# Performance work log

Measured on AMD Instinct MI355X. Metric: run time of the kernel, lower is better.

The kernel has to match this reference:

```python
import jax, jax.numpy as jnp
import numpy as np
from jax import lax

B, CIN, COUT, K, H, W, SDIM = 16, 256, 256, 3, 64, 64, 512


def setup_inputs() -> dict:
    key = jax.random.key(0)
    k1, k2, k3, k4 = jax.random.split(key, 4)
    return {
        "x": jax.random.normal(k1, (B, CIN, H, W), jnp.float32),
        "style": jax.random.normal(k2, (B, SDIM), jnp.float32),
        "weight": jax.random.normal(k3, (COUT, CIN, K, K), jnp.float32),
        "style_w": jax.random.normal(k4, (SDIM, CIN), jnp.float32) * (1.0 / np.sqrt(SDIM)),
        "style_b": jnp.zeros((CIN,), jnp.float32),
    }


def reference(x, style, weight, style_w, style_b):
    b, cin, h, w_sz = x.shape
    cout, _, k, _ = weight.shape
    mod_scale = 1.0 / np.sqrt(cin * k * k)
    # style projection: [B, CIN]
    s = style @ style_w + style_b
    # modulate: [B, COUT, CIN, K, K]
    wmod = weight[None] * s[:, None, :, None, None] * mod_scale
    # demodulate over (cin, kh, kw)
    demod = lax.rsqrt(jnp.sum(wmod * wmod, axis=(2, 3, 4)) + 1e-8)  # [B, COUT]
    wmod = wmod * demod[:, :, None, None, None]
    # per-sample conv (groups=batch equivalent) via vmap
    def conv1(xb, wb):
        # xb: [CIN, H, W], wb: [COUT, CIN, K, K]
        return lax.conv_general_dilated(
            xb[None], wb, window_strides=(1, 1), padding=[(1, 1), (1, 1)],
            dimension_numbers=("NCHW", "OIHW", "NCHW"))[0]
    return jax.vmap(conv1)(x, wmod)  # [B, COUT, H, W]
```

## Files before the change

### kernel.cpp

```cpp
#include <hip/hip_runtime.h>
#include <hip/hip_bf16.h>

#define BB 16
#define CIN 256
#define COUT 256
#define HH 64
#define WW 64
#define SDIM 512

typedef __attribute__((ext_vector_type(8))) short bf16x8;
typedef __attribute__((ext_vector_type(4))) float f32x4;

static __device__ __forceinline__ short f2bf(float v) {
    __hip_bfloat16 h = __float2bfloat16(v);
    return *reinterpret_cast<short*>(&h);
}

__global__ void style_proj_kernel(const float* __restrict__ style,
                                  const float* __restrict__ style_w,
                                  const float* __restrict__ style_b,
                                  float* __restrict__ s) {
    __shared__ float red[3][64];
    int l    = threadIdx.x & 63;
    int part = threadIdx.x >> 6;
    int ci   = blockIdx.x * 64 + l;
    int b    = blockIdx.y;
    float acc = 0.f;
    const float* st = style + b * SDIM + part * (SDIM / 4);
    const float* W  = style_w + (size_t)(part * (SDIM / 4)) * CIN + ci;
#pragma unroll 4
    for (int k = 0; k < SDIM / 4; ++k) acc += st[k] * W[(size_t)k * CIN];
    if (part) red[part - 1][l] = acc;
    __syncthreads();
    if (part == 0)
        s[b * CIN + ci] = acc + red[0][l] + red[1][l] + red[2][l] + style_b[ci];
}

__global__ void wprep_kernel(const float* __restrict__ w,
                             __hip_bfloat16* __restrict__ wT,
                             float* __restrict__ wsq) {
    int co = blockIdx.x;
    int ci = threadIdx.x;
    const float* wp = w + ((size_t)co * CIN + ci) * 9;
    float acc = 0.f;
#pragma unroll
    for (int k = 0; k < 9; ++k) {
        float v = wp[k];
        acc += v * v;
        wT[((size_t)co * 9 + k) * CIN + ci] = __float2bfloat16(v);
    }
    wsq[co * CIN + ci] = acc;
}

__global__ void demod_kernel(const float* __restrict__ wsq,
                             const float* __restrict__ s,
                             float* __restrict__ demod) {
    int b    = blockIdx.y;
    int co   = blockIdx.x * 4 + (threadIdx.x >> 6);
    int lane = threadIdx.x & 63;
    float acc = 0.f;
#pragma unroll
    for (int j = 0; j < CIN / 64; ++j) {
        int ci = j * 64 + lane;
        float sv = s[b * CIN + ci];
        acc += wsq[co * CIN + ci] * sv * sv;
    }
#pragma unroll
    for (int off = 32; off > 0; off >>= 1)
        acc += __shfl_down(acc, off, 64);
    if (lane == 0)
        demod[b * COUT + co] = rsqrtf(acc * (1.0f / (CIN * 9)) + 1e-8f);
}

__global__ void xmod_kernel(const float* __restrict__ x,
                            const float* __restrict__ s,
                            __hip_bfloat16* __restrict__ xm) {
    int px = threadIdx.x & 63;
    int y  = blockIdx.x * 4 + (threadIdx.x >> 6);
    int g  = blockIdx.y;
    int b  = blockIdx.z;
    const float* xp = x + (((size_t)(b * CIN + g * 8)) * HH + y) * WW + px;
    const float4* sp = (const float4*)(s + b * CIN + g * 8);
    float4 s0 = sp[0], s1 = sp[1];
    float sv[8] = {s0.x, s0.y, s0.z, s0.w, s1.x, s1.y, s1.z, s1.w};
    bf16x8 v;
#pragma unroll
    for (int c = 0; c < 8; ++c) v[c] = f2bf(xp[(size_t)c * (HH * WW)] * sv[c]);
    *(bf16x8*)(xm + ((((size_t)(b * 32 + g)) * HH + y) * WW + px) * 8) = v;
}

__device__ __forceinline__ void stage_dma(__hip_bfloat16* xs,
                                          const __hip_bfloat16* __restrict__ xm,
                                          int b, int cc, int Y0, int lane,
                                          int wave) {
#pragma unroll
    for (int i = 0; i < 10; ++i) {
        int u = wave * 10 + i;
        int r = u >> 2, q = u & 3;
        int y = Y0 - 1 + r;
        if ((unsigned)y < (unsigned)HH) {
            __hip_bfloat16* dst = xs + (u * 66 + 1) * 8;
            const __hip_bfloat16* src =
                xm + ((((size_t)(b * 32 + cc * 4 + q)) * HH + y) * WW + lane) * 8;
            __builtin_amdgcn_global_load_lds(
                (const __attribute__((address_space(1))) void*)src,
                (__attribute__((address_space(3))) void*)dst, 16, 0, 0);
        }
    }
}

__device__ __forceinline__ void load_af(bf16x8 (&af)[2][9],
                                        const __hip_bfloat16* __restrict__ wb,
                                        int cc) {
#pragma unroll
    for (int k = 0; k < 9; ++k) {
        af[0][k] = *(const bf16x8*)(wb + (size_t)k * CIN + cc * 32);
        af[1][k] = *(const bf16x8*)(wb + (size_t)(16 * 9 + k) * CIN + cc * 32);
    }
}

__global__ __launch_bounds__(256, 2) void conv_mfma_kernel(
    const __hip_bfloat16* __restrict__ xm, const __hip_bfloat16* __restrict__ wT,
    const float* __restrict__ wsq, const float* __restrict__ s,
    float* __restrict__ out) {
    __shared__ __hip_bfloat16 xs[40 * 66 * 8];
    __shared__ float dls[64];

    int tid  = threadIdx.x;
    int lane = tid & 63;
    int wave = tid >> 6;
    int wco  = wave >> 1;
    int rp   = wave & 1;
    int n    = lane & 15;
    int quad = lane >> 4;

    int Y0  = blockIdx.x * 8;
    int co0 = blockIdx.y * 64;
    int b   = blockIdx.z;

    const bf16x8 zv = (bf16x8){0, 0, 0, 0, 0, 0, 0, 0};
    if (tid < 80) {
        int rowq = tid >> 1, col = (tid & 1) * 65;
        *(bf16x8*)(&xs[(rowq * 66 + col) * 8]) = zv;
    }
    if (Y0 == 0) {
        for (int c = tid; c < 264; c += 256)
            *(bf16x8*)(&xs[c * 8]) = zv;
    }
    if (Y0 + 8 == HH) {
        for (int c = tid; c < 264; c += 256)
            *(bf16x8*)(&xs[(36 * 66 + c) * 8]) = zv;
    }

    stage_dma(xs, xm, b, 0, Y0, lane, wave);

    const __hip_bfloat16* wb =
        wT + ((size_t)(co0 + wco * 32 + n) * 9) * CIN + quad * 8;
    bf16x8 af[2][9];
    load_af(af, wb, 0);

    {
        int colco = tid >> 2, part = tid & 3;
        float dacc = 0.f;
        const float* wrow = wsq + (size_t)(co0 + colco) * CIN + part * 64;
        const float* srow = s + b * CIN + part * 64;
#pragma unroll 8
        for (int i = 0; i < 64; ++i) {
            float sv = srow[i];
            dacc += wrow[i] * sv * sv;
        }
        dacc += __shfl_down(dacc, 2, 64);
        dacc += __shfl_down(dacc, 1, 64);
        if (part == 0)
            dls[colco] = rsqrtf(dacc * (1.0f / (CIN * 9)) + 1e-8f);
    }

    f32x4 acc[4][2][4];
#pragma unroll
    for (int wr = 0; wr < 4; ++wr)
#pragma unroll
        for (int m = 0; m < 2; ++m)
#pragma unroll
            for (int j = 0; j < 4; ++j) acc[wr][m][j] = (f32x4){0.f, 0.f, 0.f, 0.f};

    __syncthreads();

    for (int cc = 0; cc < 8; ++cc) {
#pragma unroll
        for (int r6 = 0; r6 < 6; ++r6) {
            int rr = rp * 4 + r6;
#pragma unroll
            for (int dx = 0; dx < 3; ++dx) {
#pragma unroll
                for (int j = 0; j < 4; ++j) {
                    bf16x8 bv = *(const bf16x8*)(
                        xs + ((rr * 4 + quad) * 66 + j * 16 + n + dx) * 8);
#pragma unroll
                    for (int wr = 0; wr < 4; ++wr) {
                        int dy = r6 - wr;
                        if (dy >= 0 && dy <= 2) {
                            acc[wr][0][j] = __builtin_amdgcn_mfma_f32_16x16x32_bf16(
                                af[0][dy * 3 + dx], bv, acc[wr][0][j], 0, 0, 0);
                            acc[wr][1][j] = __builtin_amdgcn_mfma_f32_16x16x32_bf16(
                                af[1][dy * 3 + dx], bv, acc[wr][1][j], 0, 0, 0);
                        }
                    }
                }
            }
        }
        if (cc < 7) {
            __syncthreads();
            stage_dma(xs, xm, b, cc + 1, Y0, lane, wave);
            load_af(af, wb, cc + 1);
            __syncthreads();
        }
    }

    const float ms = 1.0f / 48.0f;
#pragma unroll
    for (int wr = 0; wr < 4; ++wr) {
        int gy = Y0 + rp * 4 + wr;
#pragma unroll
        for (int m = 0; m < 2; ++m) {
            int cl = wco * 32 + m * 16 + quad * 4;
            int cobase = co0 + cl;
            float d0 = dls[cl + 0] * ms;
            float d1 = dls[cl + 1] * ms;
            float d2 = dls[cl + 2] * ms;
            float d3 = dls[cl + 3] * ms;
#pragma unroll
            for (int j = 0; j < 4; ++j) {
                int gx = j * 16 + n;
                size_t o = ((size_t)(b * COUT + cobase) * HH + gy) * WW + gx;
                out[o]                       = acc[wr][m][j][0] * d0;
                out[o + (size_t)HH * WW]     = acc[wr][m][j][1] * d1;
                out[o + (size_t)2 * HH * WW] = acc[wr][m][j][2] * d2;
                out[o + (size_t)3 * HH * WW] = acc[wr][m][j][3] * d3;
            }
        }
    }
}

__device__ __forceinline__ void stage_tile(
    __hip_bfloat16* __restrict__ xsb,
    const float* __restrict__ x, const float* __restrict__ s,
    int b, int cc, int Y0, int lane, int wave) {
#pragma unroll
    for (int i = 0; i < 6; ++i) {
        int u = wave * 6 + i;
        int r = u >> 2, quad = u & 3;
        int y = Y0 - 1 + r;
        bf16x8 wv = (bf16x8){0, 0, 0, 0, 0, 0, 0, 0};
        if ((unsigned)y < (unsigned)HH) {
            const float* base =
                x + (((size_t)(b * CIN + cc * 32 + quad * 8)) * HH + y) * WW + lane;
            const float4* sp = (const float4*)(s + b * CIN + cc * 32 + quad * 8);
            float4 s0 = sp[0], s1 = sp[1];
            float sv[8] = {s0.x, s0.y, s0.z, s0.w, s1.x, s1.y, s1.z, s1.w};
#pragma unroll
            for (int c = 0; c < 8; ++c)
                wv[c] = f2bf(base[(size_t)c * (HH * WW)] * sv[c]);
        }
        *(bf16x8*)(xsb + (((r * 4 + quad) * 66) + 1 + lane) * 8) = wv;
        if (lane < 2) {
            bf16x8 z = (bf16x8){0, 0, 0, 0, 0, 0, 0, 0};
            *(bf16x8*)(xsb + (((r * 4 + quad) * 66) + lane * 65) * 8) = z;
        }
    }
}

__global__ __launch_bounds__(256, 2) void conv_mfma_fb(
    const float* __restrict__ x, const __hip_bfloat16* __restrict__ wT,
    const float* __restrict__ s, const float* __restrict__ demod,
    float* __restrict__ out) {
    __shared__ __hip_bfloat16 xs[2][6 * 4 * 66 * 8];

    int tid  = threadIdx.x;
    int lane = tid & 63;
    int wave = tid >> 6;
    int wco  = wave >> 1;
    int rp   = wave & 1;
    int n    = lane & 15;
    int quad = lane >> 4;

    int Y0  = blockIdx.x * 4;
    int co0 = blockIdx.y * 64;
    int b   = blockIdx.z;

    f32x4 acc[2][2][4];
#pragma unroll
    for (int wr = 0; wr < 2; ++wr)
#pragma unroll
        for (int m = 0; m < 2; ++m)
#pragma unroll
            for (int j = 0; j < 4; ++j) acc[wr][m][j] = (f32x4){0.f, 0.f, 0.f, 0.f};

    const __hip_bfloat16* wb =
        wT + ((size_t)(co0 + wco * 32 + n) * 9) * CIN + quad * 8;

    stage_tile(xs[0], x, s, b, 0, Y0, lane, wave);
    __syncthreads();

    for (int cc = 0; cc < 8; ++cc) {
        int cur = cc & 1;
        if (cc < 7) stage_tile(xs[cur ^ 1], x, s, b, cc + 1, Y0, lane, wave);

        bf16x8 af[2][9];
#pragma unroll
        for (int k = 0; k < 9; ++k) {
            af[0][k] = *(const bf16x8*)(wb + ((size_t)k) * CIN + cc * 32);
            af[1][k] = *(const bf16x8*)(wb + ((size_t)(16 * 9 + k)) * CIN + cc * 32);
        }

        const __hip_bfloat16* xb = xs[cur];
#pragma unroll
        for (int r4 = 0; r4 < 4; ++r4) {
            int rr = rp * 2 + r4;
#pragma unroll
            for (int dx = 0; dx < 3; ++dx) {
#pragma unroll
                for (int j = 0; j < 4; ++j) {
                    bf16x8 bv = *(const bf16x8*)(
                        xb + (((rr * 4 + quad) * 66) + j * 16 + n + dx) * 8);
                    if (r4 <= 2) {
                        acc[0][0][j] = __builtin_amdgcn_mfma_f32_16x16x32_bf16(
                            af[0][r4 * 3 + dx], bv, acc[0][0][j], 0, 0, 0);
                        acc[0][1][j] = __builtin_amdgcn_mfma_f32_16x16x32_bf16(
                            af[1][r4 * 3 + dx], bv, acc[0][1][j], 0, 0, 0);
                    }
                    if (r4 >= 1) {
                        acc[1][0][j] = __builtin_amdgcn_mfma_f32_16x16x32_bf16(
                            af[0][(r4 - 1) * 3 + dx], bv, acc[1][0][j], 0, 0, 0);
                        acc[1][1][j] = __builtin_amdgcn_mfma_f32_16x16x32_bf16(
                            af[1][(r4 - 1) * 3 + dx], bv, acc[1][1][j], 0, 0, 0);
                    }
                }
            }
        }
        __syncthreads();
    }

    const float ms = 1.0f / 48.0f;
#pragma unroll
    for (int wr = 0; wr < 2; ++wr) {
        int gy = Y0 + rp * 2 + wr;
#pragma unroll
        for (int m = 0; m < 2; ++m) {
            int cobase = co0 + wco * 32 + m * 16 + quad * 4;
            float d0 = demod[b * COUT + cobase + 0] * ms;
            float d1 = demod[b * COUT + cobase + 1] * ms;
            float d2 = demod[b * COUT + cobase + 2] * ms;
            float d3 = demod[b * COUT + cobase + 3] * ms;
#pragma unroll
            for (int j = 0; j < 4; ++j) {
                int gx = j * 16 + n;
                size_t o = ((size_t)(b * COUT + cobase) * HH + gy) * WW + gx;
                out[o]                       = acc[wr][m][j][0] * d0;
                out[o + (size_t)HH * WW]     = acc[wr][m][j][1] * d1;
                out[o + (size_t)2 * HH * WW] = acc[wr][m][j][2] * d2;
                out[o + (size_t)3 * HH * WW] = acc[wr][m][j][3] * d3;
            }
        }
    }
}

extern "C" void kernel_launch(void* const* d_in, const int* in_sizes, int n_in,
                              void* d_out, int out_size, void* d_ws, size_t ws_size,
                              hipStream_t stream) {
    const float* x       = (const float*)d_in[0];
    const float* style   = (const float*)d_in[1];
    const float* weight  = (const float*)d_in[2];
    const float* style_w = (const float*)d_in[3];
    const float* style_b = (const float*)d_in[4];
    float* out = (float*)d_out;

    float* s     = (float*)d_ws;
    float* wsq   = s + BB * CIN;
    float* demod = wsq + COUT * CIN;
    __hip_bfloat16* wT = (__hip_bfloat16*)(demod + BB * COUT);
    __hip_bfloat16* xm = wT + (size_t)COUT * 9 * CIN;

    size_t need = (size_t)(BB * CIN + COUT * CIN + BB * COUT) * sizeof(float) +
                  (size_t)COUT * 9 * CIN * sizeof(__hip_bfloat16) +
                  (size_t)BB * CIN * HH * WW * sizeof(__hip_bfloat16);

    style_proj_kernel<<<dim3(CIN / 64, BB), 256, 0, stream>>>(style, style_w,
                                                              style_b, s);
    wprep_kernel<<<COUT, CIN, 0, stream>>>(weight, wT, wsq);

    if (ws_size >= need) {
        xmod_kernel<<<dim3(HH / 4, CIN / 8, BB), 256, 0, stream>>>(x, s, xm);
        conv_mfma_kernel<<<dim3(HH / 8, COUT / 64, BB), 256, 0, stream>>>(
            xm, wT, wsq, s, out);
    } else {
        demod_kernel<<<dim3(COUT / 4, BB), 256, 0, stream>>>(wsq, s, demod);
        conv_mfma_fb<<<dim3(HH / 4, COUT / 64, BB), 256, 0, stream>>>(
            x, wT, s, demod, out);
    }
}
```

Baseline: 216.7 us.

## Read pre-padded activations straight from global memory instead of LDS staging

The xmod kernel now writes a zero-padded 66x66 bf16 layout, so the conv kernel can read B fragments directly from global memory (through cache) instead of staging tiles into LDS with two barriers per channel chunk. The style projection and weight prep kernels are merged into one launch, and weight fragments are loaded at the top of each chunk. This removes LDS traffic and block-level syncs, but each fragment is now a global or L2 load with longer latency and no explicit overlap with the MFMAs.

```diff
diff --git a/kernel.cpp b/kernel.cpp
--- a/kernel.cpp
+++ b/kernel.cpp
@@ -11,45 +11,51 @@
 typedef __attribute__((ext_vector_type(8))) short bf16x8;
 typedef __attribute__((ext_vector_type(4))) float f32x4;
 
+#define XROW 66
+#define XPLANE (XROW * XROW)
+
 static __device__ __forceinline__ short f2bf(float v) {
     __hip_bfloat16 h = __float2bfloat16(v);
     return *reinterpret_cast<short*>(&h);
 }
 
-__global__ void style_proj_kernel(const float* __restrict__ style,
-                                  const float* __restrict__ style_w,
-                                  const float* __restrict__ style_b,
-                                  float* __restrict__ s) {
+__global__ void prep_kernel(const float* __restrict__ style,
+                            const float* __restrict__ style_w,
+                            const float* __restrict__ style_b,
+                            const float* __restrict__ weight,
+                            float* __restrict__ s,
+                            __hip_bfloat16* __restrict__ wT,
+                            float* __restrict__ wsq) {
     __shared__ float red[3][64];
-    int l    = threadIdx.x & 63;
-    int part = threadIdx.x >> 6;
-    int ci   = blockIdx.x * 64 + l;
-    int b    = blockIdx.y;
-    float acc = 0.f;
-    const float* st = style + b * SDIM + part * (SDIM / 4);
-    const float* W  = style_w + (size_t)(part * (SDIM / 4)) * CIN + ci;
+    int bx = blockIdx.x;
+    if (bx < 64) {
+        int l    = threadIdx.x & 63;
+        int part = threadIdx.x >> 6;
+        int ci   = (bx & 3) * 64 + l;
+        int b    = bx >> 2;
+        float acc = 0.f;
+        const float* st = style + b * SDIM + part * (SDIM / 4);
+        const float* W  = style_w + (size_t)(part * (SDIM / 4)) * CIN + ci;
 #pragma unroll 4
-    for (int k = 0; k < SDIM / 4; ++k) acc += st[k] * W[(size_t)k * CIN];
-    if (part) red[part - 1][l] = acc;
-    __syncthreads();
-    if (part == 0)
-        s[b * CIN + ci] = acc + red[0][l] + red[1][l] + red[2][l] + style_b[ci];
-}
-
-__global__ void wprep_kernel(const float* __restrict__ w,
-                             __hip_bfloat16* __restrict__ wT,
-                             float* __restrict__ wsq) {
-    int co = blockIdx.x;
-    int ci = threadIdx.x;
-    const float* wp = w + ((size_t)co * CIN + ci) * 9;
-    float acc = 0.f;
-#pragma unroll
-    for (int k = 0; k < 9; ++k) {
-        float v = wp[k];
-        acc += v * v;
-        wT[((size_t)co * 9 + k) * CIN + ci] = __float2bfloat16(v);
-    }
-    wsq[co * CIN + ci] = acc;
+        for (int k = 0; k < SDIM / 4; ++k) acc += st[k] * W[(size_t)k * CIN];
+        if (part) red[part - 1][l] = acc;
+        __syncthreads();
+        if (part == 0)
+            s[b * CIN + ci] =
+                acc + red[0][l] + red[1][l] + red[2][l] + style_b[ci];
+    } else {
+        int co = bx - 64;
+        int ci = threadIdx.x;
+        const float* wp = weight + ((size_t)co * CIN + ci) * 9;
+        float acc = 0.f;
+#pragma unroll
+        for (int k = 0; k < 9; ++k) {
+            float v = wp[k];
+            acc += v * v;
+            wT[((size_t)co * 9 + k) * CIN + ci] = __float2bfloat16(v);
+        }
+        wsq[co * CIN + ci] = acc;
+    }
 }
 
 __global__ void demod_kernel(const float* __restrict__ wsq,
@@ -76,46 +82,30 @@
                             const float* __restrict__ s,
                             __hip_bfloat16* __restrict__ xm) {
     int px = threadIdx.x & 63;
-    int y  = blockIdx.x * 4 + (threadIdx.x >> 6);
-    int g  = blockIdx.y;
-    int b  = blockIdx.z;
-    const float* xp = x + (((size_t)(b * CIN + g * 8)) * HH + y) * WW + px;
-    const float4* sp = (const float4*)(s + b * CIN + g * 8);
-    float4 s0 = sp[0], s1 = sp[1];
-    float sv[8] = {s0.x, s0.y, s0.z, s0.w, s1.x, s1.y, s1.z, s1.w};
-    bf16x8 v;
-#pragma unroll
-    for (int c = 0; c < 8; ++c) v[c] = f2bf(xp[(size_t)c * (HH * WW)] * sv[c]);
-    *(bf16x8*)(xm + ((((size_t)(b * 32 + g)) * HH + y) * WW + px) * 8) = v;
-}
-
-__device__ __forceinline__ void stage_dma(__hip_bfloat16* xs,
-                                          const __hip_bfloat16* __restrict__ xm,
-                                          int b, int cc, int Y0, int lane,
-                                          int wave) {
-#pragma unroll
-    for (int i = 0; i < 10; ++i) {
-        int u = wave * 10 + i;
-        int r = u >> 2, q = u & 3;
-        int y = Y0 - 1 + r;
-        if ((unsigned)y < (unsigned)HH) {
-            __hip_bfloat16* dst = xs + (u * 66 + 1) * 8;
-            const __hip_bfloat16* src =
-                xm + ((((size_t)(b * 32 + cc * 4 + q)) * HH + y) * WW + lane) * 8;
-            __builtin_amdgcn_global_load_lds(
-                (const __attribute__((address_space(1))) void*)src,
-                (__attribute__((address_space(3))) void*)dst, 16, 0, 0);
-        }
-    }
-}
-
-__device__ __forceinline__ void load_af(bf16x8 (&af)[2][9],
-                                        const __hip_bfloat16* __restrict__ wb,
-                                        int cc) {
-#pragma unroll
-    for (int k = 0; k < 9; ++k) {
-        af[0][k] = *(const bf16x8*)(wb + (size_t)k * CIN + cc * 32);
-        af[1][k] = *(const bf16x8*)(wb + (size_t)(16 * 9 + k) * CIN + cc * 32);
+    int yy = blockIdx.x * 4 + (threadIdx.x >> 6);
+    if (yy >= XROW) return;
+    int g = blockIdx.y;
+    int b = blockIdx.z;
+    bf16x8 v = (bf16x8){0, 0, 0, 0, 0, 0, 0, 0};
+    if (yy >= 1 && yy <= HH) {
+        const float* xp =
+            x + (((size_t)(b * CIN + g * 8)) * HH + (yy - 1)) * WW + px;
+        const float4* sp = (const float4*)(s + b * CIN + g * 8);
+        float4 s0 = sp[0], s1 = sp[1];
+        float sv[8] = {s0.x, s0.y, s0.z, s0.w, s1.x, s1.y, s1.z, s1.w};
+#pragma unroll
+        for (int c = 0; c < 8; ++c) v[c] = f2bf(xp[(size_t)c * (HH * WW)] * sv[c]);
+    }
+    __hip_bfloat16* row =
+        xm + (((size_t)(b * 32 + g) * XROW + yy) * XROW) * 8;
+    *(bf16x8*)(row + (px + 1) * 8) = v;
+    if (px == 0) {
+        bf16x8 z = (bf16x8){0, 0, 0, 0, 0, 0, 0, 0};
+        *(bf16x8*)(row) = z;
+    }
+    if (px == 63) {
+        bf16x8 z = (bf16x8){0, 0, 0, 0, 0, 0, 0, 0};
+        *(bf16x8*)(row + 65 * 8) = z;
     }
 }
 
@@ -123,7 +113,6 @@
     const __hip_bfloat16* __restrict__ xm, const __hip_bfloat16* __restrict__ wT,
     const float* __restrict__ wsq, const float* __restrict__ s,
     float* __restrict__ out) {
-    __shared__ __hip_bfloat16 xs[40 * 66 * 8];
     __shared__ float dls[64];
 
     int tid  = threadIdx.x;
@@ -137,27 +126,6 @@
     int Y0  = blockIdx.x * 8;
     int co0 = blockIdx.y * 64;
     int b   = blockIdx.z;
-
-    const bf16x8 zv = (bf16x8){0, 0, 0, 0, 0, 0, 0, 0};
-    if (tid < 80) {
-        int rowq = tid >> 1, col = (tid & 1) * 65;
-        *(bf16x8*)(&xs[(rowq * 66 + col) * 8]) = zv;
-    }
-    if (Y0 == 0) {
-        for (int c = tid; c < 264; c += 256)
-            *(bf16x8*)(&xs[c * 8]) = zv;
-    }
-    if (Y0 + 8 == HH) {
-        for (int c = tid; c < 264; c += 256)
-            *(bf16x8*)(&xs[(36 * 66 + c) * 8]) = zv;
-    }
-
-    stage_dma(xs, xm, b, 0, Y0, lane, wave);
-
-    const __hip_bfloat16* wb =
-        wT + ((size_t)(co0 + wco * 32 + n) * 9) * CIN + quad * 8;
-    bf16x8 af[2][9];
-    load_af(af, wb, 0);
 
     {
         int colco = tid >> 2, part = tid & 3;
@@ -175,6 +143,15 @@
             dls[colco] = rsqrtf(dacc * (1.0f / (CIN * 9)) + 1e-8f);
     }
 
+    const __hip_bfloat16* wb =
+        wT + ((size_t)(co0 + wco * 32 + n) * 9) * CIN + quad * 8;
+
+    const bf16x8* bp[6];
+#pragma unroll
+    for (int r6 = 0; r6 < 6; ++r6)
+        bp[r6] = (const bf16x8*)(xm +
+            (((size_t)(b * 32 + quad) * XROW + (Y0 + rp * 4 + r6)) * XROW + n) * 8);
+
     f32x4 acc[4][2][4];
 #pragma unroll
     for (int wr = 0; wr < 4; ++wr)
@@ -186,15 +163,19 @@
     __syncthreads();
 
     for (int cc = 0; cc < 8; ++cc) {
+        bf16x8 af[2][9];
+#pragma unroll
+        for (int k = 0; k < 9; ++k) {
+            af[0][k] = *(const bf16x8*)(wb + (size_t)k * CIN + cc * 32);
+            af[1][k] = *(const bf16x8*)(wb + (size_t)(16 * 9 + k) * CIN + cc * 32);
+        }
 #pragma unroll
         for (int r6 = 0; r6 < 6; ++r6) {
-            int rr = rp * 4 + r6;
 #pragma unroll
             for (int dx = 0; dx < 3; ++dx) {
 #pragma unroll
                 for (int j = 0; j < 4; ++j) {
-                    bf16x8 bv = *(const bf16x8*)(
-                        xs + ((rr * 4 + quad) * 66 + j * 16 + n + dx) * 8);
+                    bf16x8 bv = bp[r6][j * 16 + dx];
 #pragma unroll
                     for (int wr = 0; wr < 4; ++wr) {
                         int dy = r6 - wr;
@@ -207,12 +188,7 @@
                     }
                 }
             }
-        }
-        if (cc < 7) {
-            __syncthreads();
-            stage_dma(xs, xm, b, cc + 1, Y0, lane, wave);
-            load_af(af, wb, cc + 1);
-            __syncthreads();
+            bp[r6] += 4 * XPLANE;
         }
     }
 
@@ -382,14 +358,13 @@
 
     size_t need = (size_t)(BB * CIN + COUT * CIN + BB * COUT) * sizeof(float) +
                   (size_t)COUT * 9 * CIN * sizeof(__hip_bfloat16) +
-                  (size_t)BB * CIN * HH * WW * sizeof(__hip_bfloat16);
-
-    style_proj_kernel<<<dim3(CIN / 64, BB), 256, 0, stream>>>(style, style_w,
-                                                              style_b, s);
-    wprep_kernel<<<COUT, CIN, 0, stream>>>(weight, wT, wsq);
+                  (size_t)BB * 32 * XPLANE * 8 * sizeof(__hip_bfloat16);
+
+    prep_kernel<<<320, 256, 0, stream>>>(style, style_w, style_b, weight,
+                                         s, wT, wsq);
 
     if (ws_size >= need) {
-        xmod_kernel<<<dim3(HH / 4, CIN / 8, BB), 256, 0, stream>>>(x, s, xm);
+        xmod_kernel<<<dim3(17, CIN / 8, BB), 256, 0, stream>>>(x, s, xm);
         conv_mfma_kernel<<<dim3(HH / 8, COUT / 64, BB), 256, 0, stream>>>(
             xm, wT, wsq, s, out);
     } else {
```

After: 273.6 us. 26.2% more time.

## Fuse style projection into xmod and split conv work across eight waves

Applied to the files above, without the earlier changes.

Removes the separate style projection launch: each xmod block now computes its own eight style scales with a warp reduction, and one x-row of blocks writes s for later use. The conv kernel moves to 512 threads with eight waves, each covering two output rows instead of four. Weight fragments are loaded per dx from global inside the loop instead of being held as 18 registers, which cuts register pressure so more waves fit per CU. The cost is redundant style-projection arithmetic in every xmod block and more repeated weight loads from global/L2.

```diff
diff --git a/kernel.cpp b/kernel.cpp
--- a/kernel.cpp
+++ b/kernel.cpp
@@ -14,6 +14,199 @@
 static __device__ __forceinline__ short f2bf(float v) {
     __hip_bfloat16 h = __float2bfloat16(v);
     return *reinterpret_cast<short*>(&h);
+}
+
+__global__ void wprep_kernel(const float* __restrict__ w,
+                             __hip_bfloat16* __restrict__ wT,
+                             float* __restrict__ wsq) {
+    int co = blockIdx.x;
+    int ci = threadIdx.x;
+    const float* wp = w + ((size_t)co * CIN + ci) * 9;
+    float acc = 0.f;
+#pragma unroll
+    for (int k = 0; k < 9; ++k) {
+        float v = wp[k];
+        acc += v * v;
+        wT[((size_t)co * 9 + k) * CIN + ci] = __float2bfloat16(v);
+    }
+    wsq[co * CIN + ci] = acc;
+}
+
+__global__ void xmod_kernel(const float* __restrict__ x,
+                            const float* __restrict__ style,
+                            const float* __restrict__ style_w,
+                            const float* __restrict__ style_b,
+                            float* __restrict__ s,
+                            __hip_bfloat16* __restrict__ xm) {
+    __shared__ float sls[8];
+    int t = threadIdx.x;
+    int g = blockIdx.y, b = blockIdx.z;
+    {
+        int c = t >> 5, p = t & 31;
+        float acc = 0.f;
+        const float* st = style + b * SDIM + p * 16;
+        const float* W  = style_w + (size_t)(p * 16) * CIN + g * 8 + c;
+#pragma unroll
+        for (int i = 0; i < 16; ++i) acc += st[i] * W[(size_t)i * CIN];
+#pragma unroll
+        for (int off = 16; off; off >>= 1) acc += __shfl_down(acc, off, 32);
+        if (p == 0) {
+            float v = acc + style_b[g * 8 + c];
+            sls[c] = v;
+            if (blockIdx.x == 0) s[b * CIN + g * 8 + c] = v;
+        }
+    }
+    __syncthreads();
+    int px = t & 63;
+    int y  = blockIdx.x * 4 + (t >> 6);
+    const float* xp = x + (((size_t)(b * CIN + g * 8)) * HH + y) * WW + px;
+    bf16x8 v;
+#pragma unroll
+    for (int c = 0; c < 8; ++c) v[c] = f2bf(xp[(size_t)c * (HH * WW)] * sls[c]);
+    *(bf16x8*)(xm + ((((size_t)(b * 32 + g)) * HH + y) * WW + px) * 8) = v;
+}
+
+__device__ __forceinline__ void stage_dma8(__hip_bfloat16* xs,
+                                           const __hip_bfloat16* __restrict__ xm,
+                                           int b, int cc, int Y0, int lane,
+                                           int wave) {
+#pragma unroll
+    for (int i = 0; i < 5; ++i) {
+        int u = wave * 5 + i;
+        int y = u >> 2, g = u & 3;
+        int yr = Y0 - 1 + y;
+        if ((unsigned)yr < (unsigned)HH) {
+            __hip_bfloat16* dst = xs + (u * 66 + 1) * 8;
+            const __hip_bfloat16* src =
+                xm + ((((size_t)(b * 32 + cc * 4 + g)) * HH + yr) * WW + lane) * 8;
+            __builtin_amdgcn_global_load_lds(
+                (const __attribute__((address_space(1))) void*)src,
+                (__attribute__((address_space(3))) void*)dst, 16, 0, 0);
+        }
+    }
+}
+
+__global__ __launch_bounds__(512, 4) void conv_mfma_kernel(
+    const __hip_bfloat16* __restrict__ xm, const __hip_bfloat16* __restrict__ wT,
+    const float* __restrict__ wsq, const float* __restrict__ s,
+    float* __restrict__ out) {
+    __shared__ __hip_bfloat16 xs[40 * 66 * 8];
+    __shared__ float dls[64];
+
+    int tid  = threadIdx.x;
+    int lane = tid & 63;
+    int wave = tid >> 6;
+    int wco  = wave & 1;
+    int rq   = wave >> 1;
+    int n    = lane & 15;
+    int quad = lane >> 4;
+
+    int Y0  = blockIdx.x * 8;
+    int co0 = blockIdx.y * 64;
+    int b   = blockIdx.z;
+
+    const bf16x8 zv = (bf16x8){0, 0, 0, 0, 0, 0, 0, 0};
+    if (tid < 80) {
+        int u = tid >> 1, col = (tid & 1) * 65;
+        *(bf16x8*)(&xs[(u * 66 + col) * 8]) = zv;
+    }
+    if (Y0 == 0 && tid < 264)
+        *(bf16x8*)(&xs[tid * 8]) = zv;
+    if (Y0 + 8 == HH && tid < 264)
+        *(bf16x8*)(&xs[(36 * 66 + tid) * 8]) = zv;
+
+    stage_dma8(xs, xm, b, 0, Y0, lane, wave);
+
+    {
+        int colco = tid >> 3, part = tid & 7;
+        float dacc = 0.f;
+        const float* wrow = wsq + (size_t)(co0 + colco) * CIN + part * 32;
+        const float* srow = s + b * CIN + part * 32;
+#pragma unroll 8
+        for (int i = 0; i < 32; ++i) {
+            float sv = srow[i];
+            dacc += wrow[i] * sv * sv;
+        }
+        dacc += __shfl_down(dacc, 4, 64);
+        dacc += __shfl_down(dacc, 2, 64);
+        dacc += __shfl_down(dacc, 1, 64);
+        if (part == 0)
+            dls[colco] = rsqrtf(dacc * (1.0f / (CIN * 9)) + 1e-8f);
+    }
+
+    const __hip_bfloat16* wb =
+        wT + ((size_t)(co0 + wco * 32 + n) * 9) * CIN + quad * 8;
+
+    f32x4 acc[2][2][4];
+#pragma unroll
+    for (int wr = 0; wr < 2; ++wr)
+#pragma unroll
+        for (int m = 0; m < 2; ++m)
+#pragma unroll
+            for (int j = 0; j < 4; ++j) acc[wr][m][j] = (f32x4){0.f, 0.f, 0.f, 0.f};
+
+    __syncthreads();
+
+    for (int cc = 0; cc < 8; ++cc) {
+#pragma unroll
+        for (int dx = 0; dx < 3; ++dx) {
+            bf16x8 af[2][3];
+#pragma unroll
+            for (int m = 0; m < 2; ++m)
+#pragma unroll
+                for (int dy = 0; dy < 3; ++dy)
+                    af[m][dy] = *(const bf16x8*)(
+                        wb + (size_t)(m * 16 * 9 + dy * 3 + dx) * CIN + cc * 32);
+#pragma unroll
+            for (int r4 = 0; r4 < 4; ++r4) {
+                int rr = rq * 2 + r4;
+#pragma unroll
+                for (int j = 0; j < 4; ++j) {
+                    bf16x8 bv = *(const bf16x8*)(
+                        &xs[((rr * 4 + quad) * 66 + j * 16 + n + dx) * 8]);
+#pragma unroll
+                    for (int wr = 0; wr < 2; ++wr) {
+                        int dy = r4 - wr;
+                        if (dy >= 0 && dy <= 2) {
+                            acc[wr][0][j] = __builtin_amdgcn_mfma_f32_16x16x32_bf16(
+                                af[0][dy], bv, acc[wr][0][j], 0, 0, 0);
+                            acc[wr][1][j] = __builtin_amdgcn_mfma_f32_16x16x32_bf16(
+                                af[1][dy], bv, acc[wr][1][j], 0, 0, 0);
+                        }
+                    }
+                }
+            }
+        }
+        __syncthreads();
+        if (cc < 7) {
+            stage_dma8(xs, xm, b, cc + 1, Y0, lane, wave);
+            __syncthreads();
+        }
+    }
+
+    const float ms = 1.0f / 48.0f;
+#pragma unroll
+    for (int wr = 0; wr < 2; ++wr) {
+        int gy = Y0 + rq * 2 + wr;
+#pragma unroll
+        for (int m = 0; m < 2; ++m) {
+            int cl = wco * 32 + m * 16 + quad * 4;
+            int cobase = co0 + cl;
+            float d0 = dls[cl + 0] * ms;
+            float d1 = dls[cl + 1] * ms;
+            float d2 = dls[cl + 2] * ms;
+            float d3 = dls[cl + 3] * ms;
+#pragma unroll
+            for (int j = 0; j < 4; ++j) {
+                int gx = j * 16 + n;
+                size_t o = ((size_t)(b * COUT + cobase) * HH + gy) * WW + gx;
+                out[o]                       = acc[wr][m][j][0] * d0;
+                out[o + (size_t)HH * WW]     = acc[wr][m][j][1] * d1;
+                out[o + (size_t)2 * HH * WW] = acc[wr][m][j][2] * d2;
+                out[o + (size_t)3 * HH * WW] = acc[wr][m][j][3] * d3;
+            }
+        }
+    }
 }
 
 __global__ void style_proj_kernel(const float* __restrict__ style,
@@ -36,22 +229,6 @@
         s[b * CIN + ci] = acc + red[0][l] + red[1][l] + red[2][l] + style_b[ci];
 }
 
-__global__ void wprep_kernel(const float* __restrict__ w,
-                             __hip_bfloat16* __restrict__ wT,
-                             float* __restrict__ wsq) {
-    int co = blockIdx.x;
-    int ci = threadIdx.x;
-    const float* wp = w + ((size_t)co * CIN + ci) * 9;
-    float acc = 0.f;
-#pragma unroll
-    for (int k = 0; k < 9; ++k) {
-        float v = wp[k];
-        acc += v * v;
-        wT[((size_t)co * 9 + k) * CIN + ci] = __float2bfloat16(v);
-    }
-    wsq[co * CIN + ci] = acc;
-}
-
 __global__ void demod_kernel(const float* __restrict__ wsq,
                              const float* __restrict__ s,
                              float* __restrict__ demod) {
@@ -70,175 +247,6 @@
         acc += __shfl_down(acc, off, 64);
     if (lane == 0)
         demod[b * COUT + co] = rsqrtf(acc * (1.0f / (CIN * 9)) + 1e-8f);
-}
-
-__global__ void xmod_kernel(const float* __restrict__ x,
-                            const float* __restrict__ s,
-                            __hip_bfloat16* __restrict__ xm) {
-    int px = threadIdx.x & 63;
-    int y  = blockIdx.x * 4 + (threadIdx.x >> 6);
-    int g  = blockIdx.y;
-    int b  = blockIdx.z;
-    const float* xp = x + (((size_t)(b * CIN + g * 8)) * HH + y) * WW + px;
-    const float4* sp = (const float4*)(s + b * CIN + g * 8);
-    float4 s0 = sp[0], s1 = sp[1];
-    float sv[8] = {s0.x, s0.y, s0.z, s0.w, s1.x, s1.y, s1.z, s1.w};
-    bf16x8 v;
-#pragma unroll
-    for (int c = 0; c < 8; ++c) v[c] = f2bf(xp[(size_t)c * (HH * WW)] * sv[c]);
-    *(bf16x8*)(xm + ((((size_t)(b * 32 + g)) * HH + y) * WW + px) * 8) = v;
-}
-
-__device__ __forceinline__ void stage_dma(__hip_bfloat16* xs,
-                                          const __hip_bfloat16* __restrict__ xm,
-                                          int b, int cc, int Y0, int lane,
-                                          int wave) {
-#pragma unroll
-    for (int i = 0; i < 10; ++i) {
-        int u = wave * 10 + i;
-        int r = u >> 2, q = u & 3;
-        int y = Y0 - 1 + r;
-        if ((unsigned)y < (unsigned)HH) {
-            __hip_bfloat16* dst = xs + (u * 66 + 1) * 8;
-            const __hip_bfloat16* src =
-                xm + ((((size_t)(b * 32 + cc * 4 + q)) * HH + y) * WW + lane) * 8;
-            __builtin_amdgcn_global_load_lds(
-                (const __attribute__((address_space(1))) void*)src,
-                (__attribute__((address_space(3))) void*)dst, 16, 0, 0);
-        }
-    }
-}
-
-__device__ __forceinline__ void load_af(bf16x8 (&af)[2][9],
-                                        const __hip_bfloat16* __restrict__ wb,
-                                        int cc) {
-#pragma unroll
-    for (int k = 0; k < 9; ++k) {
-        af[0][k] = *(const bf16x8*)(wb + (size_t)k * CIN + cc * 32);
-        af[1][k] = *(const bf16x8*)(wb + (size_t)(16 * 9 + k) * CIN + cc * 32);
-    }
-}
-
-__global__ __launch_bounds__(256, 2) void conv_mfma_kernel(
-    const __hip_bfloat16* __restrict__ xm, const __hip_bfloat16* __restrict__ wT,
-    const float* __restrict__ wsq, const float* __restrict__ s,
-    float* __restrict__ out) {
-    __shared__ __hip_bfloat16 xs[40 * 66 * 8];
-    __shared__ float dls[64];
-
-    int tid  = threadIdx.x;
-    int lane = tid & 63;
-    int wave = tid >> 6;
-    int wco  = wave >> 1;
-    int rp   = wave & 1;
-    int n    = lane & 15;
-    int quad = lane >> 4;
-
-    int Y0  = blockIdx.x * 8;
-    int co0 = blockIdx.y * 64;
-    int b   = blockIdx.z;
-
-    const bf16x8 zv = (bf16x8){0, 0, 0, 0, 0, 0, 0, 0};
-    if (tid < 80) {
-        int rowq = tid >> 1, col = (tid & 1) * 65;
-        *(bf16x8*)(&xs[(rowq * 66 + col) * 8]) = zv;
-    }
-    if (Y0 == 0) {
-        for (int c = tid; c < 264; c += 256)
-            *(bf16x8*)(&xs[c * 8]) = zv;
-    }
-    if (Y0 + 8 == HH) {
-        for (int c = tid; c < 264; c += 256)
-            *(bf16x8*)(&xs[(36 * 66 + c) * 8]) = zv;
-    }
-
-    stage_dma(xs, xm, b, 0, Y0, lane, wave);
-
-    const __hip_bfloat16* wb =
-        wT + ((size_t)(co0 + wco * 32 + n) * 9) * CIN + quad * 8;
-    bf16x8 af[2][9];
-    load_af(af, wb, 0);
-
-    {
-        int colco = tid >> 2, part = tid & 3;
-        float dacc = 0.f;
-        const float* wrow = wsq + (size_t)(co0 + colco) * CIN + part * 64;
-        const float* srow = s + b * CIN + part * 64;
-#pragma unroll 8
-        for (int i = 0; i < 64; ++i) {
-            float sv = srow[i];
-            dacc += wrow[i] * sv * sv;
-        }
-        dacc += __shfl_down(dacc, 2, 64);
-        dacc += __shfl_down(dacc, 1, 64);
-        if (part == 0)
-            dls[colco] = rsqrtf(dacc * (1.0f / (CIN * 9)) + 1e-8f);
-    }
-
-    f32x4 acc[4][2][4];
-#pragma unroll
-    for (int wr = 0; wr < 4; ++wr)
-#pragma unroll
-        for (int m = 0; m < 2; ++m)
-#pragma unroll
-            for (int j = 0; j < 4; ++j) acc[wr][m][j] = (f32x4){0.f, 0.f, 0.f, 0.f};
-
-    __syncthreads();
-
-    for (int cc = 0; cc < 8; ++cc) {
-#pragma unroll
-        for (int r6 = 0; r6 < 6; ++r6) {
-            int rr = rp * 4 + r6;
-#pragma unroll
-            for (int dx = 0; dx < 3; ++dx) {
-#pragma unroll
-                for (int j = 0; j < 4; ++j) {
-                    bf16x8 bv = *(const bf16x8*)(
-                        xs + ((rr * 4 + quad) * 66 + j * 16 + n + dx) * 8);
-#pragma unroll
-                    for (int wr = 0; wr < 4; ++wr) {
-                        int dy = r6 - wr;
-                        if (dy >= 0 && dy <= 2) {
-                            acc[wr][0][j] = __builtin_amdgcn_mfma_f32_16x16x32_bf16(
-                                af[0][dy * 3 + dx], bv, acc[wr][0][j], 0, 0, 0);
-                            acc[wr][1][j] = __builtin_amdgcn_mfma_f32_16x16x32_bf16(
-                                af[1][dy * 3 + dx], bv, acc[wr][1][j], 0, 0, 0);
-                        }
-                    }
-                }
-            }
-        }
-        if (cc < 7) {
-            __syncthreads();
-            stage_dma(xs, xm, b, cc + 1, Y0, lane, wave);
-            load_af(af, wb, cc + 1);
-            __syncthreads();
-        }
-    }
-
-    const float ms = 1.0f / 48.0f;
-#pragma unroll
-    for (int wr = 0; wr < 4; ++wr) {
-        int gy = Y0 + rp * 4 + wr;
-#pragma unroll
-        for (int m = 0; m < 2; ++m) {
-            int cl = wco * 32 + m * 16 + quad * 4;
-            int cobase = co0 + cl;
-            float d0 = dls[cl + 0] * ms;
-            float d1 = dls[cl + 1] * ms;
-            float d2 = dls[cl + 2] * ms;
-            float d3 = dls[cl + 3] * ms;
-#pragma unroll
-            for (int j = 0; j < 4; ++j) {
-                int gx = j * 16 + n;
-                size_t o = ((size_t)(b * COUT + cobase) * HH + gy) * WW + gx;
-                out[o]                       = acc[wr][m][j][0] * d0;
-                out[o + (size_t)HH * WW]     = acc[wr][m][j][1] * d1;
-                out[o + (size_t)2 * HH * WW] = acc[wr][m][j][2] * d2;
-                out[o + (size_t)3 * HH * WW] = acc[wr][m][j][3] * d3;
-            }
-        }
-    }
 }
 
 __device__ __forceinline__ void stage_tile(
@@ -384,15 +392,16 @@
                   (size_t)COUT * 9 * CIN * sizeof(__hip_bfloat16) +
                   (size_t)BB * CIN * HH * WW * sizeof(__hip_bfloat16);
 
-    style_proj_kernel<<<dim3(CIN / 64, BB), 256, 0, stream>>>(style, style_w,
-                                                              style_b, s);
     wprep_kernel<<<COUT, CIN, 0, stream>>>(weight, wT, wsq);
 
     if (ws_size >= need) {
-        xmod_kernel<<<dim3(HH / 4, CIN / 8, BB), 256, 0, stream>>>(x, s, xm);
-        conv_mfma_kernel<<<dim3(HH / 8, COUT / 64, BB), 256, 0, stream>>>(
+        xmod_kernel<<<dim3(HH / 4, CIN / 8, BB), 256, 0, stream>>>(
+            x, style, style_w, style_b, s, xm);
+        conv_mfma_kernel<<<dim3(HH / 8, COUT / 64, BB), 512, 0, stream>>>(
             xm, wT, wsq, s, out);
     } else {
+        style_proj_kernel<<<dim3(CIN / 64, BB), 256, 0, stream>>>(
+            style, style_w, style_b, s);
         demod_kernel<<<dim3(COUT / 4, BB), 256, 0, stream>>>(wsq, s, demod);
         conv_mfma_fb<<<dim3(HH / 4, COUT / 64, BB), 256, 0, stream>>>(
             x, wT, s, demod, out);
```

Result: slower. 293.7 us (+35.5%).
